# Optimization experiments

Hardware: AMD Instinct MI355X
Metric: run time of the kernel (lower is better)

## Reference

```python
import jax, jax.numpy as jnp
import numpy as np

D_MODEL = 1024
NUM_HEADS = 16
D_K = D_MODEL // NUM_HEADS
NEG_INF = -1e9


def setup_inputs() -> dict:
    key = jax.random.key(0)
    ks = jax.random.split(key, 12)
    B, S = 2, 2048
    scale = 1.0 / np.sqrt(D_MODEL)
    inp = {
        "q": jax.random.normal(ks[0], (B, S, D_MODEL), jnp.float32),
        "k": jax.random.normal(ks[1], (B, S, D_MODEL), jnp.float32),
        "v": jax.random.normal(ks[2], (B, S, D_MODEL), jnp.float32),
        "mask": jnp.ones((B, S), jnp.int32),
        "W_q": jax.random.normal(ks[3], (D_MODEL, D_MODEL), jnp.float32) * scale,
        "b_q": jnp.zeros((D_MODEL,), jnp.float32),
        "W_k": jax.random.normal(ks[4], (D_MODEL, D_MODEL), jnp.float32) * scale,
        "b_k": jnp.zeros((D_MODEL,), jnp.float32),
        "W_v": jax.random.normal(ks[5], (D_MODEL, D_MODEL), jnp.float32) * scale,
        "b_v": jnp.zeros((D_MODEL,), jnp.float32),
        "W_o": jax.random.normal(ks[6], (D_MODEL, D_MODEL), jnp.float32) * scale,
        "b_o": jnp.zeros((D_MODEL,), jnp.float32),
    }
    return inp


def reference(q, k, v, mask, W_q, b_q, W_k, b_k, W_v, b_v, W_o, b_o):
    B, S, _ = q.shape
    def proj(x, W, b):
        # [B,S,D] -> [B,H,S,d_k]
        y = x @ W.T + b
        return y.reshape(B, -1, NUM_HEADS, D_K).transpose(0, 2, 1, 3)
    qh = proj(q, W_q, b_q)
    kh = proj(k, W_k, b_k)
    vh = proj(v, W_v, b_v)
    scores = jnp.einsum("bhqd,bhkd->bhqk", qh, kh) / jnp.sqrt(jnp.float32(D_K))
    # 2D mask [B,S_k] -> broadcast over heads and query positions
    m = mask[:, None, None, :]
    scores = jnp.where(m == 0, jnp.float32(NEG_INF), scores)
    attn = jax.nn.softmax(scores, axis=-1)
    # dropout is identity at inference
    context = jnp.einsum("bhqk,bhkd->bhqd", attn, vh)
    context = context.transpose(0, 2, 1, 3).reshape(B, S, D_MODEL)
    return context @ W_o.T + b_o
```

## Files before the change

### kernel.cpp

```cpp
#include <hip/hip_runtime.h>
#include <hip/hip_bf16.h>
#include <cstdint>
#include <cstddef>

#define DMODEL 1024
#define NHEADS 16
#define DK 64
#define SEQ 2048
#define BATCH 2
#define NT (SEQ / 32)

typedef short bf16x8 __attribute__((ext_vector_type(8)));
typedef float f32x4 __attribute__((ext_vector_type(4)));
typedef float f32x16 __attribute__((ext_vector_type(16)));
typedef unsigned int u32x2 __attribute__((ext_vector_type(2)));
typedef unsigned int u32x4 __attribute__((ext_vector_type(4)));

typedef const __attribute__((address_space(1))) void* gas_ptr;
typedef __attribute__((address_space(3))) void* las_ptr;

__device__ __forceinline__ void gld_lds16(const void* g, void* l) {
    __builtin_amdgcn_global_load_lds((gas_ptr)g, (las_ptr)l, 16, 0, 0);
}

__device__ __forceinline__ ushort f2bf_u(float f) {
    uint32_t x = __float_as_uint(f);
    x += 0x7fff + ((x >> 16) & 1);
    return (ushort)(x >> 16);
}

__global__ __launch_bounds__(256) void cast_all(
        const float* __restrict__ q, const float* __restrict__ k,
        const float* __restrict__ v, const float* __restrict__ Wq,
        const float* __restrict__ Wk, const float* __restrict__ Wv,
        const float* __restrict__ Wo,
        ushort* __restrict__ qb, ushort* __restrict__ kb, ushort* __restrict__ vb,
        ushort* __restrict__ Wqb, ushort* __restrict__ Wkb,
        ushort* __restrict__ Wvb, ushort* __restrict__ Wob) {
    int bid = blockIdx.x;
    const float* src; ushort* dst; int base;
    if      (bid <  4096) { src = q;  dst = qb;  base = bid; }
    else if (bid <  8192) { src = k;  dst = kb;  base = bid - 4096; }
    else if (bid < 12288) { src = v;  dst = vb;  base = bid - 8192; }
    else if (bid < 13312) { src = Wq; dst = Wqb; base = bid - 12288; }
    else if (bid < 14336) { src = Wk; dst = Wkb; base = bid - 13312; }
    else if (bid < 15360) { src = Wv; dst = Wvb; base = bid - 14336; }
    else                  { src = Wo; dst = Wob; base = bid - 15360; }
    int i = base * 1024 + threadIdx.x * 4;
    float4 f = *reinterpret_cast<const float4*>(src + i);
    ushort4 o;
    o.x = f2bf_u(f.x); o.y = f2bf_u(f.y); o.z = f2bf_u(f.z); o.w = f2bf_u(f.w);
    *reinterpret_cast<ushort4*>(dst + i) = o;
}

__global__ __launch_bounds__(256) void mask2bias(
        const int* __restrict__ m, float* __restrict__ mb) {
    int i = (blockIdx.x * 256 + threadIdx.x) * 4;
    int4 mk = *reinterpret_cast<const int4*>(m + i);
    float4 o;
    o.x = mk.x ? 0.f : -1e9f;
    o.y = mk.y ? 0.f : -1e9f;
    o.z = mk.z ? 0.f : -1e9f;
    o.w = mk.w ? 0.f : -1e9f;
    *reinterpret_cast<float4*>(mb + i) = o;
}

__global__ __launch_bounds__(256) void gemm_qkv(
        const ushort* __restrict__ A,
        const ushort* __restrict__ Wall,
        const float* __restrict__ bq, const float* __restrict__ bk,
        const float* __restrict__ bv,
        ushort* __restrict__ Qh, ushort* __restrict__ Kh, ushort* __restrict__ Vt) {
    __shared__ ushort As[128 * 32];
    __shared__ ushort Bs[128 * 32];
    const int tid = threadIdx.x;
    const int w = tid >> 6, lane = tid & 63;
    const int lr = lane & 15, lg = lane >> 4;
    int lid = (blockIdx.x & 7) * 96 + (blockIdx.x >> 3);
    const int tMg = (lid >> 3) << 7;
    const int tN  = (lid & 7) << 7;
    const int g   = tMg >> 12;
    const ushort* W = Wall + (size_t)g * 1024 * 1024;
    const float* bias = (g == 0) ? bq : (g == 1 ? bk : bv);
    const int wr = (w >> 1) * 64, wc = (w & 1) * 64;

    f32x4 acc[4][4] = {};

    const int c0 = (w * 2 + 0) * 64 + lane;
    const int c1 = (w * 2 + 1) * 64 + lane;
    const ushort* gA0 = A + (size_t)(tMg + (c0 >> 2)) * 1024 + (c0 & 3) * 8;
    const ushort* gA1 = A + (size_t)(tMg + (c1 >> 2)) * 1024 + (c1 & 3) * 8;
    const ushort* gB0 = W + (size_t)(tN + (c0 >> 2)) * 1024 + (c0 & 3) * 8;
    const ushort* gB1 = W + (size_t)(tN + (c1 >> 2)) * 1024 + (c1 & 3) * 8;
    ushort* lA0 = As + (w * 2 + 0) * 512;
    ushort* lA1 = As + (w * 2 + 1) * 512;
    ushort* lB0 = Bs + (w * 2 + 0) * 512;
    ushort* lB1 = Bs + (w * 2 + 1) * 512;

    for (int k0 = 0; k0 < 1024; k0 += 32) {
        gld_lds16(gA0 + k0, lA0);
        gld_lds16(gA1 + k0, lA1);
        gld_lds16(gB0 + k0, lB0);
        gld_lds16(gB1 + k0, lB1);
        __syncthreads();

        bf16x8 af[4], bfr[4];
#pragma unroll
        for (int i = 0; i < 4; i++)
            af[i] = *(const bf16x8*)(As + (wr + i * 16 + lr) * 32 + lg * 8);
#pragma unroll
        for (int i = 0; i < 4; i++)
            bfr[i] = *(const bf16x8*)(Bs + (wc + i * 16 + lr) * 32 + lg * 8);
#pragma unroll
        for (int mi = 0; mi < 4; mi++)
#pragma unroll
            for (int ni = 0; ni < 4; ni++)
                acc[mi][ni] = __builtin_amdgcn_mfma_f32_16x16x32_bf16(
                    af[mi], bfr[ni], acc[mi][ni], 0, 0, 0);
        __syncthreads();
    }

#pragma unroll
    for (int mi = 0; mi < 4; mi++) {
        const int row0 = tMg + wr + mi * 16 + lg * 4;
#pragma unroll
        for (int ni = 0; ni < 4; ni++) {
            const int col = tN + wc + ni * 16 + lr;
            const int h = col >> 6, d = col & (DK - 1);
            const float bvv = bias[col];
#pragma unroll
            for (int r = 0; r < 4; r++) {
                float vv = acc[mi][ni][r] + bvv;
                int mloc = (row0 + r) & 4095;
                int b = mloc >> 11, s = mloc & (SEQ - 1);
                if (g == 0)
                    Qh[(((size_t)(b * NHEADS + h) * SEQ + s) * DK) + d] = f2bf_u(vv);
                else if (g == 1)
                    Kh[(((size_t)(b * NHEADS + h) * SEQ + s) * DK) + d] = f2bf_u(vv);
                else
                    Vt[(((size_t)(b * NHEADS + h) * DK + d) * SEQ) + s] = f2bf_u(vv);
            }
        }
    }
}

__global__ __launch_bounds__(256) void gemm_out(
        const ushort* __restrict__ A,
        const ushort* __restrict__ W,
        const float* __restrict__ bias,
        float* __restrict__ out, int M, int N, int K) {
    __shared__ ushort As[64 * 32];
    __shared__ ushort Bs[128 * 32];
    const int tid = threadIdx.x;
    const int w = tid >> 6, lane = tid & 63;
    const int lr = lane & 15, lg = lane >> 4;
    const int nTiles = N >> 7;
    const int cpx = gridDim.x >> 3;
    int lid = (blockIdx.x & 7) * cpx + (blockIdx.x >> 3);
    const int tM = (lid / nTiles) << 6;
    const int tN = (lid % nTiles) << 7;
    const int wr = (w >> 1) * 32, wc = (w & 1) * 64;

    f32x4 acc[2][4] = {};

    const int cA = w * 64 + lane;
    const int cB0 = w * 128 + lane;
    const int cB1 = w * 128 + 64 + lane;
    const ushort* gA  = A + (size_t)(tM + (cA  >> 2)) * K + (cA  & 3) * 8;
    const ushort* gB0 = W + (size_t)(tN + (cB0 >> 2)) * K + (cB0 & 3) * 8;
    const ushort* gB1 = W + (size_t)(tN + (cB1 >> 2)) * K + (cB1 & 3) * 8;
    ushort* lA  = As + w * 512;
    ushort* lB0 = Bs + w * 1024;
    ushort* lB1 = Bs + w * 1024 + 512;

    for (int k0 = 0; k0 < K; k0 += 32) {
        gld_lds16(gA  + k0, lA);
        gld_lds16(gB0 + k0, lB0);
        gld_lds16(gB1 + k0, lB1);
        __syncthreads();

        bf16x8 af[2], bfr[4];
#pragma unroll
        for (int i = 0; i < 2; i++)
            af[i] = *(const bf16x8*)(As + (wr + i * 16 + lr) * 32 + lg * 8);
#pragma unroll
        for (int i = 0; i < 4; i++)
            bfr[i] = *(const bf16x8*)(Bs + (wc + i * 16 + lr) * 32 + lg * 8);
#pragma unroll
        for (int mi = 0; mi < 2; mi++)
#pragma unroll
            for (int ni = 0; ni < 4; ni++)
                acc[mi][ni] = __builtin_amdgcn_mfma_f32_16x16x32_bf16(
                    af[mi], bfr[ni], acc[mi][ni], 0, 0, 0);
        __syncthreads();
    }

#pragma unroll
    for (int mi = 0; mi < 2; mi++) {
        const int row0 = tM + wr + mi * 16 + lg * 4;
#pragma unroll
        for (int ni = 0; ni < 4; ni++) {
            const int col = tN + wc + ni * 16 + lr;
            const float bv = bias[col];
#pragma unroll
            for (int r = 0; r < 4; r++)
                out[(size_t)(row0 + r) * N + col] = acc[mi][ni][r] + bv;
        }
    }
}

#define SCALE2 0.18033688011120542f

__device__ __forceinline__ bf16x8 pack_pa(const float* p) {
    uint a, b, c, d;
    asm("v_cvt_pk_bf16_f32 %0, %1, %2" : "=v"(a) : "v"(p[0]), "v"(p[1]));
    asm("v_cvt_pk_bf16_f32 %0, %1, %2" : "=v"(b) : "v"(p[4]), "v"(p[5]));
    asm("v_cvt_pk_bf16_f32 %0, %1, %2" : "=v"(c) : "v"(p[2]), "v"(p[3]));
    asm("v_cvt_pk_bf16_f32 %0, %1, %2" : "=v"(d) : "v"(p[6]), "v"(p[7]));
    asm("v_permlane32_swap_b32 %0, %1" : "+v"(a), "+v"(b));
    asm("v_permlane32_swap_b32 %0, %1" : "+v"(c), "+v"(d));
    union { u32x4 u; bf16x8 h; } cv;
    cv.u = (u32x4){a, c, b, d};
    return cv.h;
}

__device__ __forceinline__ float xmax32(float x) {
    u32x2 r = __builtin_amdgcn_permlane32_swap(__float_as_uint(x), __float_as_uint(x), false, false);
    return fmaxf(__uint_as_float(r[0]), __uint_as_float(r[1]));
}
__device__ __forceinline__ float xadd32(float x) {
    u32x2 r = __builtin_amdgcn_permlane32_swap(__float_as_uint(x), __float_as_uint(x), false, false);
    return __uint_as_float(r[0]) + __uint_as_float(r[1]);
}

__global__ __launch_bounds__(256) void attn_fwd32(
        const ushort* __restrict__ Qh, const ushort* __restrict__ Kh,
        const ushort* __restrict__ Vt, const float* __restrict__ mbias,
        ushort* __restrict__ ctx) {
    __shared__ ushort Ks[2][2048];
    __shared__ ushort Vs[2][2048];
    __shared__ float  Ml[SEQ];

    const int tid = threadIdx.x;
    const int w = tid >> 6;
    const int l = tid & 63;
    const int q32 = l & 31, hi = l >> 5;
    const int q7 = l & 7;

    int lid = (blockIdx.x & 7) * 64 + (blockIdx.x >> 3);
    const int qblk = lid & 15;
    const int bh = lid >> 4;
    const int b = bh >> 4;
    const int h = bh & 15;
    const int q0 = qblk * 128 + w * 32;

    const ushort* Qp = Qh + (size_t)bh * SEQ * DK + (size_t)(q0 + q32) * DK + hi * 8;
    const ushort* Kg = Kh + (size_t)bh * SEQ * DK;
    const ushort* Vg = Vt + (size_t)bh * DK * SEQ;

    const int srow = tid >> 3;
    const int scs  = (tid & 7) ^ (srow & 7);
    const ushort* Ksrc = Kg + (size_t)srow * DK + scs * 8;
    const ushort* Vsrc = Vg + (size_t)(srow + ((scs & 4) << 3)) * SEQ + (scs & 3) * 8;

    {
        const float* mg = mbias + (size_t)b * SEQ;
        gld_lds16(mg + tid * 4,        &Ml[w * 256]);
        gld_lds16(mg + 1024 + tid * 4, &Ml[1024 + w * 256]);
    }

    auto STAGE = [&](int buf, int t) {
        const int kv0 = t * 32;
        gld_lds16(Ksrc + (size_t)kv0 * DK, &Ks[buf][w * 512]);
        gld_lds16(Vsrc + kv0,              &Vs[buf][w * 512]);
    };

    bf16x8 qf[4];
#pragma unroll
    for (int dc = 0; dc < 4; dc++)
        qf[dc] = *(const bf16x8*)(Qp + dc * 16);

    f32x16 c0 = {}, c1 = {};
    float m2 = -1e30f, lrun = 0.f;

    STAGE(0, 0);
    __syncthreads();

    for (int t = 0; t < NT; ++t) {
        const int buf = t & 1;
        if (t + 1 < NT) STAGE(buf ^ 1, t + 1);

        const ushort* Kb = &Ks[buf][0];
        const ushort* Vb = &Vs[buf][0];

        bf16x8 kf[4];
#pragma unroll
        for (int dc = 0; dc < 4; dc++)
            kf[dc] = *(const bf16x8*)(Kb + q32 * 64 + (((dc * 2 + hi) ^ q7) * 8));
        f32x16 s = {};
        __builtin_amdgcn_s_setprio(1);
#pragma unroll
        for (int dc = 0; dc < 4; dc++)
            s = __builtin_amdgcn_mfma_f32_32x32x16_bf16(kf[dc], qf[dc], s, 0, 0, 0);
        __builtin_amdgcn_s_setprio(0);

        const int kv0 = t * 32;
        float4 mb[4];
#pragma unroll
        for (int g = 0; g < 4; g++)
            mb[g] = *reinterpret_cast<const float4*>(&Ml[kv0 + g * 8 + hi * 4]);
        float p[16];
#pragma unroll
        for (int r = 0; r < 16; r++)
            p[r] = fmaf(s[r], SCALE2, reinterpret_cast<const float*>(&mb[r >> 2])[r & 3]);

        float m01 = fmaxf(p[0], p[1]),   m23 = fmaxf(p[2], p[3]);
        float m45 = fmaxf(p[4], p[5]),   m67 = fmaxf(p[6], p[7]);
        float m89 = fmaxf(p[8], p[9]),   mab = fmaxf(p[10], p[11]);
        float mcd = fmaxf(p[12], p[13]), mef = fmaxf(p[14], p[15]);
        float pm = fmaxf(fmaxf(fmaxf(m01, m23), fmaxf(m45, m67)),
                         fmaxf(fmaxf(m89, mab), fmaxf(mcd, mef)));
        pm = xmax32(pm);
        if (__any(pm - m2 > 8.0f)) {
            float mnew = fmaxf(m2, pm);
            float alpha = __builtin_amdgcn_exp2f(m2 - mnew);
            m2 = mnew; lrun *= alpha;
#pragma unroll
            for (int r = 0; r < 16; r++) {
                float aT = __shfl(alpha, (r & 3) + 8 * (r >> 2) + 4 * hi);
                c0[r] *= aT; c1[r] *= aT;
            }
        }

        float rs = 0.f;
#pragma unroll
        for (int r = 0; r < 16; r++) {
            p[r] = __builtin_amdgcn_exp2f(p[r] - m2);
            rs += p[r];
        }
        lrun += xadd32(rs);

        bf16x8 pa0 = pack_pa(p);
        bf16x8 pa1 = pack_pa(p + 8);

        bf16x8 vc[4];
#pragma unroll
        for (int dt = 0; dt < 2; dt++)
#pragma unroll
            for (int ks = 0; ks < 2; ks++)
                vc[dt * 2 + ks] = *(const bf16x8*)(Vb + q32 * 64 + (((dt * 4 + ks * 2 + hi) ^ q7) * 8));

        __builtin_amdgcn_s_setprio(1);
        c0 = __builtin_amdgcn_mfma_f32_32x32x16_bf16(pa0, vc[0], c0, 0, 0, 0);
        c1 = __builtin_amdgcn_mfma_f32_32x32x16_bf16(pa0, vc[2], c1, 0, 0, 0);
        c0 = __builtin_amdgcn_mfma_f32_32x32x16_bf16(pa1, vc[1], c0, 0, 0, 0);
        c1 = __builtin_amdgcn_mfma_f32_32x32x16_bf16(pa1, vc[3], c1, 0, 0, 0);
        __builtin_amdgcn_s_setprio(0);

        __syncthreads();
    }

    float rl = 1.0f / lrun;
#pragma unroll
    for (int r = 0; r < 16; r++) {
        int crow = (r & 3) + 8 * (r >> 2) + 4 * hi;
        float rlT = __shfl(rl, crow);
        int qq = q0 + crow;
        size_t base = (size_t)(b * SEQ + qq) * DMODEL + h * DK;
        ctx[base + q32]      = f2bf_u(c0[r] * rlT);
        ctx[base + 32 + q32] = f2bf_u(c1[r] * rlT);
    }
}

extern "C" void kernel_launch(void* const* d_in, const int* in_sizes, int n_in,
                              void* d_out, int out_size, void* d_ws, size_t ws_size,
                              hipStream_t stream) {
    const float* q    = (const float*)d_in[0];
    const float* k    = (const float*)d_in[1];
    const float* v    = (const float*)d_in[2];
    const int*   mask = (const int*)d_in[3];
    const float* Wq   = (const float*)d_in[4];
    const float* bq   = (const float*)d_in[5];
    const float* Wk   = (const float*)d_in[6];
    const float* bk   = (const float*)d_in[7];
    const float* Wv   = (const float*)d_in[8];
    const float* bv   = (const float*)d_in[9];
    const float* Wo   = (const float*)d_in[10];
    const float* bo   = (const float*)d_in[11];

    char* ws = (char*)d_ws;
    ushort* qb   = (ushort*)(ws + (size_t)0);
    ushort* kb   = (ushort*)(ws + ((size_t)8  << 20));
    ushort* vb   = (ushort*)(ws + ((size_t)16 << 20));
    ushort* Wqb  = (ushort*)(ws + ((size_t)24 << 20));
    ushort* Wkb  = (ushort*)(ws + ((size_t)26 << 20));
    ushort* Wvb  = (ushort*)(ws + ((size_t)28 << 20));
    ushort* Wob  = (ushort*)(ws + ((size_t)30 << 20));
    ushort* Qh   = (ushort*)(ws + ((size_t)32 << 20));
    ushort* Kh   = (ushort*)(ws + ((size_t)40 << 20));
    ushort* Vt   = (ushort*)(ws + ((size_t)48 << 20));
    ushort* ctxb = (ushort*)(ws + ((size_t)56 << 20));
    float*  mbias = (float*)(ws + (size_t)0);

    cast_all<<<16384, 256, 0, stream>>>(q, k, v, Wq, Wk, Wv, Wo,
                                        qb, kb, vb, Wqb, Wkb, Wvb, Wob);

    gemm_qkv<<<768, 256, 0, stream>>>(qb, Wqb, bq, bk, bv, Qh, Kh, Vt);

    mask2bias<<<BATCH * SEQ / 1024, 256, 0, stream>>>(mask, mbias);

    attn_fwd32<<<BATCH * NHEADS * (SEQ / 128), 256, 0, stream>>>(Qh, Kh, Vt, mbias, ctxb);

    const int M = BATCH * SEQ;
    gemm_out<<<(M / 64) * (DMODEL / 128), 256, 0, stream>>>(
        ctxb, Wob, bo, (float*)d_out, M, DMODEL, DMODEL);
}
```

Before: 152.1 us.

## Process 64 keys per attention iteration and defer row-sum cross-lane reduction

The flash-attention loop now stages and processes two 32-key sub-tiles per iteration, halving the number of barriers, max reductions and rescale checks per key. The two score MFMA chains are interleaved for more instruction-level parallelism. The per-iteration cross-half sum of the softmax denominator is moved to a single reduction after the loop. In exchange, LDS use doubles and register pressure rises, which may reduce occupancy.

```diff
diff --git a/kernel.cpp b/kernel.cpp
--- a/kernel.cpp
+++ b/kernel.cpp
@@ -8,7 +8,7 @@
 #define DK 64
 #define SEQ 2048
 #define BATCH 2
-#define NT (SEQ / 32)
+#define NT2 (SEQ / 64)
 
 typedef short bf16x8 __attribute__((ext_vector_type(8)));
 typedef float f32x4 __attribute__((ext_vector_type(4)));
@@ -237,8 +237,8 @@
         const ushort* __restrict__ Qh, const ushort* __restrict__ Kh,
         const ushort* __restrict__ Vt, const float* __restrict__ mbias,
         ushort* __restrict__ ctx) {
-    __shared__ ushort Ks[2][2048];
-    __shared__ ushort Vs[2][2048];
+    __shared__ ushort Ks[2][2][2048];
+    __shared__ ushort Vs[2][2][2048];
     __shared__ float  Ml[SEQ];
 
     const int tid = threadIdx.x;
@@ -270,9 +270,11 @@
     }
 
     auto STAGE = [&](int buf, int t) {
-        const int kv0 = t * 32;
-        gld_lds16(Ksrc + (size_t)kv0 * DK, &Ks[buf][w * 512]);
-        gld_lds16(Vsrc + kv0,              &Vs[buf][w * 512]);
+        const int kv0 = t * 64;
+        gld_lds16(Ksrc + (size_t)kv0 * DK,        &Ks[buf][0][w * 512]);
+        gld_lds16(Ksrc + (size_t)(kv0 + 32) * DK, &Ks[buf][1][w * 512]);
+        gld_lds16(Vsrc + kv0,                     &Vs[buf][0][w * 512]);
+        gld_lds16(Vsrc + kv0 + 32,                &Vs[buf][1][w * 512]);
     };
 
     bf16x8 qf[4];
@@ -286,40 +288,43 @@
     STAGE(0, 0);
     __syncthreads();
 
-    for (int t = 0; t < NT; ++t) {
+    for (int t = 0; t < NT2; ++t) {
         const int buf = t & 1;
-        if (t + 1 < NT) STAGE(buf ^ 1, t + 1);
-
-        const ushort* Kb = &Ks[buf][0];
-        const ushort* Vb = &Vs[buf][0];
-
-        bf16x8 kf[4];
+        if (t + 1 < NT2) STAGE(buf ^ 1, t + 1);
+
+        const int kv0 = t * 64;
+
+        bf16x8 kf0[4], kf1[4];
 #pragma unroll
         for (int dc = 0; dc < 4; dc++)
-            kf[dc] = *(const bf16x8*)(Kb + q32 * 64 + (((dc * 2 + hi) ^ q7) * 8));
-        f32x16 s = {};
+            kf0[dc] = *(const bf16x8*)(&Ks[buf][0][q32 * 64 + (((dc * 2 + hi) ^ q7) * 8)]);
+#pragma unroll
+        for (int dc = 0; dc < 4; dc++)
+            kf1[dc] = *(const bf16x8*)(&Ks[buf][1][q32 * 64 + (((dc * 2 + hi) ^ q7) * 8)]);
+        f32x16 s0 = {}, s1 = {};
         __builtin_amdgcn_s_setprio(1);
 #pragma unroll
-        for (int dc = 0; dc < 4; dc++)
-            s = __builtin_amdgcn_mfma_f32_32x32x16_bf16(kf[dc], qf[dc], s, 0, 0, 0);
+        for (int dc = 0; dc < 4; dc++) {
+            s0 = __builtin_amdgcn_mfma_f32_32x32x16_bf16(kf0[dc], qf[dc], s0, 0, 0, 0);
+            s1 = __builtin_amdgcn_mfma_f32_32x32x16_bf16(kf1[dc], qf[dc], s1, 0, 0, 0);
+        }
         __builtin_amdgcn_s_setprio(0);
 
-        const int kv0 = t * 32;
-        float4 mb[4];
-#pragma unroll
-        for (int g = 0; g < 4; g++)
-            mb[g] = *reinterpret_cast<const float4*>(&Ml[kv0 + g * 8 + hi * 4]);
-        float p[16];
-#pragma unroll
-        for (int r = 0; r < 16; r++)
-            p[r] = fmaf(s[r], SCALE2, reinterpret_cast<const float*>(&mb[r >> 2])[r & 3]);
-
-        float m01 = fmaxf(p[0], p[1]),   m23 = fmaxf(p[2], p[3]);
-        float m45 = fmaxf(p[4], p[5]),   m67 = fmaxf(p[6], p[7]);
-        float m89 = fmaxf(p[8], p[9]),   mab = fmaxf(p[10], p[11]);
-        float mcd = fmaxf(p[12], p[13]), mef = fmaxf(p[14], p[15]);
-        float pm = fmaxf(fmaxf(fmaxf(m01, m23), fmaxf(m45, m67)),
-                         fmaxf(fmaxf(m89, mab), fmaxf(mcd, mef)));
+        float p0[16], p1[16];
+#pragma unroll
+        for (int g = 0; g < 4; g++) {
+            float4 mb0 = *reinterpret_cast<const float4*>(&Ml[kv0 + g * 8 + hi * 4]);
+            float4 mb1 = *reinterpret_cast<const float4*>(&Ml[kv0 + 32 + g * 8 + hi * 4]);
+#pragma unroll
+            for (int j = 0; j < 4; j++) {
+                p0[g * 4 + j] = fmaf(s0[g * 4 + j], SCALE2, reinterpret_cast<const float*>(&mb0)[j]);
+                p1[g * 4 + j] = fmaf(s1[g * 4 + j], SCALE2, reinterpret_cast<const float*>(&mb1)[j]);
+            }
+        }
+
+        float pm = fmaxf(p0[0], p1[0]);
+#pragma unroll
+        for (int r = 1; r < 16; r++) pm = fmaxf(pm, fmaxf(p0[r], p1[r]));
         pm = xmax32(pm);
         if (__any(pm - m2 > 8.0f)) {
             float mnew = fmaxf(m2, pm);
@@ -335,32 +340,41 @@
         float rs = 0.f;
 #pragma unroll
         for (int r = 0; r < 16; r++) {
-            p[r] = __builtin_amdgcn_exp2f(p[r] - m2);
-            rs += p[r];
-        }
-        lrun += xadd32(rs);
-
-        bf16x8 pa0 = pack_pa(p);
-        bf16x8 pa1 = pack_pa(p + 8);
-
-        bf16x8 vc[4];
+            p0[r] = __builtin_amdgcn_exp2f(p0[r] - m2);
+            p1[r] = __builtin_amdgcn_exp2f(p1[r] - m2);
+            rs += p0[r] + p1[r];
+        }
+        lrun += rs;
+
+        bf16x8 pa00 = pack_pa(p0);
+        bf16x8 pa01 = pack_pa(p0 + 8);
+        bf16x8 pa10 = pack_pa(p1);
+        bf16x8 pa11 = pack_pa(p1 + 8);
+
+        bf16x8 vc0[4], vc1[4];
 #pragma unroll
         for (int dt = 0; dt < 2; dt++)
 #pragma unroll
-            for (int ks = 0; ks < 2; ks++)
-                vc[dt * 2 + ks] = *(const bf16x8*)(Vb + q32 * 64 + (((dt * 4 + ks * 2 + hi) ^ q7) * 8));
+            for (int ks = 0; ks < 2; ks++) {
+                vc0[dt * 2 + ks] = *(const bf16x8*)(&Vs[buf][0][q32 * 64 + (((dt * 4 + ks * 2 + hi) ^ q7) * 8)]);
+                vc1[dt * 2 + ks] = *(const bf16x8*)(&Vs[buf][1][q32 * 64 + (((dt * 4 + ks * 2 + hi) ^ q7) * 8)]);
+            }
 
         __builtin_amdgcn_s_setprio(1);
-        c0 = __builtin_amdgcn_mfma_f32_32x32x16_bf16(pa0, vc[0], c0, 0, 0, 0);
-        c1 = __builtin_amdgcn_mfma_f32_32x32x16_bf16(pa0, vc[2], c1, 0, 0, 0);
-        c0 = __builtin_amdgcn_mfma_f32_32x32x16_bf16(pa1, vc[1], c0, 0, 0, 0);
-        c1 = __builtin_amdgcn_mfma_f32_32x32x16_bf16(pa1, vc[3], c1, 0, 0, 0);
+        c0 = __builtin_amdgcn_mfma_f32_32x32x16_bf16(pa00, vc0[0], c0, 0, 0, 0);
+        c1 = __builtin_amdgcn_mfma_f32_32x32x16_bf16(pa00, vc0[2], c1, 0, 0, 0);
+        c0 = __builtin_amdgcn_mfma_f32_32x32x16_bf16(pa01, vc0[1], c0, 0, 0, 0);
+        c1 = __builtin_amdgcn_mfma_f32_32x32x16_bf16(pa01, vc0[3], c1, 0, 0, 0);
+        c0 = __builtin_amdgcn_mfma_f32_32x32x16_bf16(pa10, vc1[0], c0, 0, 0, 0);
+        c1 = __builtin_amdgcn_mfma_f32_32x32x16_bf16(pa10, vc1[2], c1, 0, 0, 0);
+        c0 = __builtin_amdgcn_mfma_f32_32x32x16_bf16(pa11, vc1[1], c0, 0, 0, 0);
+        c1 = __builtin_amdgcn_mfma_f32_32x32x16_bf16(pa11, vc1[3], c1, 0, 0, 0);
         __builtin_amdgcn_s_setprio(0);
 
         __syncthreads();
     }
 
-    float rl = 1.0f / lrun;
+    float rl = 1.0f / xadd32(lrun);
 #pragma unroll
     for (int r = 0; r < 16; r++) {
         int crow = (r & 3) + 8 * (r >> 2) + 4 * hi;
```

Result: faster. 147.5 us (-3.0%).
